# Kernel optimization log

Hardware: AMD Instinct MI355X
Metric: run time of the kernel (lower is better)

Reference implementation:

```python
import jax, jax.numpy as jnp
import numpy as np

N, E, IN, HID, H, C, L, NC = 10000, 60000, 768, 256, 8, 256, 4, 2
EPS, SLOPE = 1e-5, 0.2

def _ln(x, g, b):
    m = x.mean(-1, keepdims=True)
    v = x.var(-1, keepdims=True)
    return (x - m) / jnp.sqrt(v + EPS) * g + b

def _gelu(x):
    return jax.nn.gelu(x, approximate=False)  # torch nn.GELU default (erf)

def setup_inputs() -> dict:
    key = jax.random.key(0)
    ks = iter(jax.random.split(key, 40))
    def p(shape, s=0.02):
        return jax.random.normal(next(ks), shape, jnp.float32) * s
    return dict(
        x=jax.random.normal(next(ks), (N, IN), jnp.float32),
        edge_index=jax.random.randint(next(ks), (2, E), 0, N, dtype=jnp.int32),
        W_in=p((HID, IN)), b_in=jnp.zeros((HID,), jnp.float32),
        virtual_node=p((1, HID)),
        Wl=p((L, H * C, HID)), bl=jnp.zeros((L, H * C), jnp.float32),
        Wr=p((L, H * C, HID)), br=jnp.zeros((L, H * C), jnp.float32),
        att=p((L, H, C)), gbias=jnp.zeros((L, HID), jnp.float32),
        V1=p((L, 2 * HID, HID)), v1b=jnp.zeros((L, 2 * HID), jnp.float32),
        V2=p((L, HID, 2 * HID)), v2b=jnp.zeros((L, HID), jnp.float32),
        U1=p((L, 2 * HID, 2 * HID)), u1b=jnp.zeros((L, 2 * HID), jnp.float32),
        U2=p((L, HID, 2 * HID)), u2b=jnp.zeros((L, HID), jnp.float32),
        g1=jnp.ones((L, HID), jnp.float32), be1=jnp.zeros((L, HID), jnp.float32),
        g2=jnp.ones((L, HID), jnp.float32), be2=jnp.zeros((L, HID), jnp.float32),
        g3=jnp.ones((L, HID), jnp.float32), be3=jnp.zeros((L, HID), jnp.float32),
        O1=p((HID, HID)), o1b=jnp.zeros((HID,), jnp.float32),
        O2=p((NC, HID)), o2b=jnp.zeros((NC,), jnp.float32),
    )

def reference(x, edge_index, W_in, b_in, virtual_node, Wl, bl, Wr, br, att, gbias,
              V1, v1b, V2, v2b, U1, u1b, U2, u2b,
              g1, be1, g2, be2, g3, be3, O1, o1b, O2, o2b):
    # add self loops (PyG add_self_loops=True)
    loops = jnp.arange(N, dtype=edge_index.dtype)
    src = jnp.concatenate([edge_index[0], loops])  # message sources j
    dst = jnp.concatenate([edge_index[1], loops])  # message targets i

    x = x @ W_in.T + b_in                      # [N, HID]
    vn = virtual_node                          # [1, HID]
    for i in range(L):
        # --- GATv2Conv (concat=False -> mean over heads), eval mode (no dropout) ---
        xl = (x @ Wl[i].T + bl[i]).reshape(N, H, C)   # source transform
        xr = (x @ Wr[i].T + br[i]).reshape(N, H, C)   # target transform
        m = jax.nn.leaky_relu(xl[src] + xr[dst], SLOPE)       # [Etot, H, C]
        e = jnp.einsum('ehc,hc->eh', m, att[i])                # [Etot, H]
        emax = jax.ops.segment_max(e, dst, num_segments=N)
        a = jnp.exp(e - emax[dst])
        denom = jax.ops.segment_sum(a, dst, num_segments=N)
        alpha = a / denom[dst]                                  # segment softmax
        agg = jax.ops.segment_sum(xl[src] * alpha[:, :, None], dst, num_segments=N)
        x_local = agg.mean(axis=1) + gbias[i]                   # [N, HID]
        x = _ln(x + x_local, g1[i], be1[i])
        # --- virtual node update ---
        vn_in = x.mean(axis=0, keepdims=True)
        vn_up = _gelu(vn_in @ V1[i].T + v1b[i]) @ V2[i].T + v2b[i]
        vn = _ln(vn + vn_up, g2[i], be2[i])
        # --- node update with broadcast VN ---
        xc = jnp.concatenate([x, jnp.broadcast_to(vn, (N, HID))], axis=1)
        xu = _gelu(xc @ U1[i].T + u1b[i]) @ U2[i].T + u2b[i]
        x = _ln(x + xu, g3[i], be3[i])
    return _gelu(x @ O1.T + o1b) @ O2.T + o2b
```

## Files before the change

kernel.cpp:

```cpp
#include <hip/hip_runtime.h>
#include <hip/hip_bf16.h>
#include <cstdint>
#include <cstddef>

#define N_NODES 10000
#define M_PAD   10112
#define N_EDGES 60000
#define ETOT    70000
#define DIM_IN  768
#define HID     256
#define NHEAD   8
#define CH      256
#define HC      2048
#define NLAYER  4
#define NCLS    2
#define EPSLN   1e-5f
#define SLOPE   0.2f
#define DEG_CAP 128

typedef __bf16 bf16;
typedef __bf16 bf16x8 __attribute__((ext_vector_type(8)));
typedef float  f32x4  __attribute__((ext_vector_type(4)));

__device__ __forceinline__ float gelu_erf(float x) {
  return 0.5f * x * (1.0f + erff(x * 0.70710678118654752f));
}

__device__ __forceinline__ void gl2lds16(const void* g, void* l) {
  __builtin_amdgcn_global_load_lds(
      (const __attribute__((address_space(1))) unsigned int*)g,
      (__attribute__((address_space(3))) unsigned int*)l,
      16, 0, 0);
}

__global__ void k_count(const int* __restrict__ ei, int* __restrict__ deg) {
  int e = blockIdx.x * 256 + threadIdx.x;
  if (e >= ETOT) return;
  int d = (e < N_EDGES) ? ei[N_EDGES + e] : (e - N_EDGES);
  atomicAdd(&deg[d], 1);
}

__global__ void k_scan(const int* __restrict__ deg, int* __restrict__ offs) {
  __shared__ int lds[1024];
  const int t = threadIdx.x;
  const int c0 = t * 10;
  int s = 0;
  #pragma unroll
  for (int q = 0; q < 10; ++q) { int idx = c0 + q; if (idx < N_NODES) s += deg[idx]; }
  lds[t] = s;
  __syncthreads();
  for (int o = 1; o < 1024; o <<= 1) {
    int v = (t >= o) ? lds[t - o] : 0;
    __syncthreads();
    lds[t] += v;
    __syncthreads();
  }
  int run = lds[t] - s;
  #pragma unroll
  for (int q = 0; q < 10; ++q) {
    int idx = c0 + q;
    if (idx < N_NODES) { offs[idx] = run; run += deg[idx]; }
  }
  if (t == 1023) offs[N_NODES] = lds[1023];
}

__global__ void k_scatter(const int* __restrict__ ei, const int* __restrict__ offs,
                          int* __restrict__ fill, int* __restrict__ adj) {
  int e = blockIdx.x * 256 + threadIdx.x;
  if (e >= ETOT) return;
  int s, d;
  if (e < N_EDGES) { s = ei[e]; d = ei[N_EDGES + e]; } else { s = e - N_EDGES; d = s; }
  int pos = offs[d] + atomicAdd(&fill[d], 1);
  adj[pos] = s;
}

__global__ void k_init_vn(const float* __restrict__ vnode, float* __restrict__ vn_cur) {
  int t = threadIdx.x;
  if (t < HID) vn_cur[t] = vnode[t];
}

__global__ void k_f2b(const float* __restrict__ src, bf16* __restrict__ dst, int n4) {
  int i = blockIdx.x * 256 + threadIdx.x;
  int stride = gridDim.x * 256;
  for (; i < n4; i += stride) {
    float4 v = reinterpret_cast<const float4*>(src)[i];
    bf16 o0 = (bf16)v.x, o1 = (bf16)v.y, o2 = (bf16)v.z, o3 = (bf16)v.w;
    ushort4 pack;
    pack.x = __builtin_bit_cast(unsigned short, o0);
    pack.y = __builtin_bit_cast(unsigned short, o1);
    pack.z = __builtin_bit_cast(unsigned short, o2);
    pack.w = __builtin_bit_cast(unsigned short, o3);
    reinterpret_cast<ushort4*>(dst)[i] = pack;
  }
}

__global__ void k_catw(const float* __restrict__ Wl, const float* __restrict__ Wr,
                       bf16* __restrict__ out) {
  int idx = blockIdx.x * 256 + threadIdx.x;
  const int total8 = NLAYER * 4096 * 256 / 8;
  if (idx >= total8) return;
  size_t flat = (size_t)idx * 8;
  int i   = (int)(flat / (4096 * 256));
  int rem = (int)(flat % (4096 * 256));
  int r = rem >> 8;
  int k = rem & 255;
  const float* src = (r < 2048)
      ? Wl + (((size_t)i * 2048 + r) << 8) + k
      : Wr + (((size_t)i * 2048 + (r - 2048)) << 8) + k;
  const float4* p4 = reinterpret_cast<const float4*>(src);
  float4 u0 = p4[0], u1 = p4[1];
  bf16x8 ov;
  ov[0]=(bf16)u0.x; ov[1]=(bf16)u0.y; ov[2]=(bf16)u0.z; ov[3]=(bf16)u0.w;
  ov[4]=(bf16)u1.x; ov[5]=(bf16)u1.y; ov[6]=(bf16)u1.z; ov[7]=(bf16)u1.w;
  reinterpret_cast<bf16x8*>(out)[idx] = ov;
}

__global__ void k_catb(const float* __restrict__ bl, const float* __restrict__ br,
                       float* __restrict__ out) {
  int idx = blockIdx.x * 256 + threadIdx.x;
  if (idx >= NLAYER * 4096) return;
  int i = idx >> 12, r = idx & 4095;
  out[idx] = (r < 2048) ? bl[i * 2048 + r] : br[i * 2048 + (r - 2048)];
}

template<int ACT, bool WB, bool WF>
__global__ __launch_bounds__(256) void k_gemm2(
    const bf16* __restrict__ A, int lda,
    const bf16* __restrict__ W, int ldw,
    const float* __restrict__ bias,
    bf16* __restrict__ Cb, float* __restrict__ Cf, int ldc,
    int M, int K, int NT)
{
  __shared__ bf16 As[2][128 * 64];
  __shared__ bf16 Bs[2][128 * 64];
  const int t = threadIdx.x;
  const int nwg = gridDim.x;
  const int qq = nwg >> 3, rr = nwg & 7;
  const int xcd = blockIdx.x & 7, loc = blockIdx.x >> 3;
  const int wg = (xcd < rr) ? (xcd * (qq + 1) + loc)
                            : (rr * (qq + 1) + (xcd - rr) * qq + loc);
  const int bm = (wg / NT) * 128;
  const int bn = (wg % NT) * 128;
  const int l = t & 63, w = t >> 6;
  const int wm = (w >> 1) * 64, wn = (w & 1) * 64;
  const int lr = l & 15, lg = l >> 4;
  const int sr = t >> 3;
  const int ps = t & 7;

  f32x4 acc[4][4];
  #pragma unroll
  for (int a = 0; a < 4; ++a)
    #pragma unroll
    for (int b = 0; b < 4; ++b) acc[a][b] = (f32x4){0.f, 0.f, 0.f, 0.f};

  auto stage = [&](int buf, int k0) {
    #pragma unroll
    for (int q = 0; q < 4; ++q) {
      int r = q * 32 + sr;
      int ls = ps ^ (r & 7);
      gl2lds16(A + (size_t)(bm + r) * lda + k0 + ls * 8, &As[buf][r * 64 + ps * 8]);
    }
    #pragma unroll
    for (int q = 0; q < 4; ++q) {
      int r = q * 32 + sr;
      int ls = ps ^ (r & 7);
      gl2lds16(W + (size_t)(bn + r) * ldw + k0 + ls * 8, &Bs[buf][r * 64 + ps * 8]);
    }
  };

  const int nt = K >> 6;
  stage(0, 0);
  __syncthreads();
  for (int kt = 0; kt < nt; ++kt) {
    if (kt + 1 < nt) stage((kt + 1) & 1, (kt + 1) << 6);
    const bf16* Ab = As[kt & 1];
    const bf16* Bb = Bs[kt & 1];
    #pragma unroll
    for (int ks = 0; ks < 2; ++ks) {
      bf16x8 af[4], bfr[4];
      #pragma unroll
      for (int mt = 0; mt < 4; ++mt) {
        int row = wm + mt * 16 + lr;
        int slot = ks * 4 + lg;
        af[mt] = *reinterpret_cast<const bf16x8*>(&Ab[row * 64 + ((slot ^ (row & 7)) * 8)]);
      }
      #pragma unroll
      for (int nt2 = 0; nt2 < 4; ++nt2) {
        int row = wn + nt2 * 16 + lr;
        int slot = ks * 4 + lg;
        bfr[nt2] = *reinterpret_cast<const bf16x8*>(&Bb[row * 64 + ((slot ^ (row & 7)) * 8)]);
      }
      #pragma unroll
      for (int mt = 0; mt < 4; ++mt)
        #pragma unroll
        for (int nt2 = 0; nt2 < 4; ++nt2)
          acc[mt][nt2] = __builtin_amdgcn_mfma_f32_16x16x32_bf16(af[mt], bfr[nt2], acc[mt][nt2], 0, 0, 0);
    }
    __syncthreads();
  }
  #pragma unroll
  for (int mt = 0; mt < 4; ++mt) {
    #pragma unroll
    for (int nt2 = 0; nt2 < 4; ++nt2) {
      int col = bn + wn + nt2 * 16 + lr;
      float bv = bias[col];
      #pragma unroll
      for (int j = 0; j < 4; ++j) {
        int row = bm + wm + mt * 16 + lg * 4 + j;
        if (row < M) {
          float vv = acc[mt][nt2][j] + bv;
          if (ACT == 1) vv = gelu_erf(vv);
          if (WB) Cb[(size_t)row * ldc + col] = (bf16)vv;
          if (WF) Cf[(size_t)row * ldc + col] = vv;
        }
      }
    }
  }
}

__global__ __launch_bounds__(256) void k_node_attn(
    float* __restrict__ x, bf16* __restrict__ xb,
    const bf16* __restrict__ xlr,
    const int* __restrict__ offs, const int* __restrict__ adj,
    const float* __restrict__ att_l, const float* __restrict__ gbias_l,
    const float* __restrict__ g_l, const float* __restrict__ b_l)
{
  __shared__ int   s_src[DEG_CAP];
  __shared__ float s_agg[HC];
  __shared__ float s_red[8];

  const int t = threadIdx.x;
  const int i = blockIdx.x;
  const int start = offs[i];
  int deg = offs[i + 1] - start;
  if (deg > DEG_CAP) deg = DEG_CAP;

  for (int j = t; j < deg; j += 256) s_src[j] = adj[start + j];

  float xr_reg[8], att_reg[8];
  {
    bf16x8 xv = *reinterpret_cast<const bf16x8*>(xlr + (size_t)i * 4096 + 2048 + 8 * t);
    #pragma unroll
    for (int q = 0; q < 8; ++q) xr_reg[q] = (float)xv[q];
    const float4* ap = reinterpret_cast<const float4*>(att_l + 8 * t);
    float4 a0 = ap[0], a1 = ap[1];
    att_reg[0]=a0.x; att_reg[1]=a0.y; att_reg[2]=a0.z; att_reg[3]=a0.w;
    att_reg[4]=a1.x; att_reg[5]=a1.y; att_reg[6]=a1.z; att_reg[7]=a1.w;
  }
  __syncthreads();

  float m = -1e30f, ssum = 0.f;
  float acc[8];
  #pragma unroll
  for (int q = 0; q < 8; ++q) acc[q] = 0.f;

  for (int j = 0; j < deg; ++j) {
    bf16x8 xv = *reinterpret_cast<const bf16x8*>(xlr + (size_t)s_src[j] * 4096 + 8 * t);
    float xf[8];
    float p = 0.f;
    #pragma unroll
    for (int q = 0; q < 8; ++q) {
      xf[q] = (float)xv[q];
      float z = xf[q] + xr_reg[q];
      z = (z > 0.f) ? z : SLOPE * z;
      p = fmaf(att_reg[q], z, p);
    }
    #pragma unroll
    for (int o = 16; o >= 1; o >>= 1) p += __shfl_xor(p, o, 32);
    if (__any(p > m)) {
      float mn = fmaxf(m, p);
      float scale = __expf(m - mn);
      ssum *= scale;
      #pragma unroll
      for (int q = 0; q < 8; ++q) acc[q] *= scale;
      m = mn;
    }
    float a = __expf(p - m);
    ssum += a;
    #pragma unroll
    for (int q = 0; q < 8; ++q) acc[q] = fmaf(a, xf[q], acc[q]);
  }
  float inv = 1.0f / ssum;
  #pragma unroll
  for (int q = 0; q < 8; ++q) s_agg[8 * t + q] = acc[q] * inv;
  __syncthreads();

  float xloc = 0.f;
  #pragma unroll
  for (int hh = 0; hh < NHEAD; ++hh) xloc += s_agg[hh * CH + t];
  xloc = xloc * (1.0f / NHEAD) + gbias_l[t];
  float r = x[(size_t)i * HID + t] + xloc;

  float s1 = r, s2 = r * r;
  #pragma unroll
  for (int o = 32; o >= 1; o >>= 1) { s1 += __shfl_xor(s1, o); s2 += __shfl_xor(s2, o); }
  if ((t & 63) == 0) { s_red[t >> 6] = s1; s_red[4 + (t >> 6)] = s2; }
  __syncthreads();
  s1 = s_red[0] + s_red[1] + s_red[2] + s_red[3];
  s2 = s_red[4] + s_red[5] + s_red[6] + s_red[7];
  float mean = s1 * (1.0f / HID);
  float var  = s2 * (1.0f / HID) - mean * mean;
  float o = (r - mean) * rsqrtf(var + EPSLN) * g_l[t] + b_l[t];
  x [(size_t)i * HID + t] = o;
  xb[(size_t)i * HID + t] = (bf16)o;
}

__global__ void k_colmean(const float* __restrict__ x, float* __restrict__ accum) {
  const int t = threadIdx.x, b = blockIdx.x;
  float s = 0.f;
  for (int r = b * 50; r < (b + 1) * 50; ++r) s += x[(size_t)r * HID + t];
  atomicAdd(&accum[t], s);
}

__global__ void k_vn_gemv1(const float* __restrict__ vn_accum,
                           const float* __restrict__ V1, const float* __restrict__ v1b,
                           float* __restrict__ z1) {
  const int o = blockIdx.x * 8 + (threadIdx.x >> 5);
  const int lane = threadIdx.x & 31;
  const float4* vp = reinterpret_cast<const float4*>(vn_accum + lane * 8);
  float4 a0 = vp[0], a1 = vp[1];
  const float4* wp = reinterpret_cast<const float4*>(V1 + (size_t)o * 256 + lane * 8);
  float4 w0 = wp[0], w1 = wp[1];
  float p = a0.x*w0.x + a0.y*w0.y + a0.z*w0.z + a0.w*w0.w
          + a1.x*w1.x + a1.y*w1.y + a1.z*w1.z + a1.w*w1.w;
  #pragma unroll
  for (int s = 16; s >= 1; s >>= 1) p += __shfl_xor(p, s, 32);
  if (lane == 0) z1[o] = gelu_erf(p * (1.0f / (float)N_NODES) + v1b[o]);
}

__global__ void k_vn_gemv2(const float* __restrict__ z1,
                           const float* __restrict__ V2, const float* __restrict__ v2b,
                           float* __restrict__ vn_up) {
  const int o = blockIdx.x * 8 + (threadIdx.x >> 5);
  const int lane = threadIdx.x & 31;
  float p = 0.f;
  #pragma unroll
  for (int c = 0; c < 4; ++c) {
    float4 a = reinterpret_cast<const float4*>(z1 + lane * 16)[c];
    float4 w = reinterpret_cast<const float4*>(V2 + (size_t)o * 512 + lane * 16)[c];
    p += a.x*w.x + a.y*w.y + a.z*w.z + a.w*w.w;
  }
  #pragma unroll
  for (int s = 16; s >= 1; s >>= 1) p += __shfl_xor(p, s, 32);
  if (lane == 0) vn_up[o] = p + v2b[o];
}

__global__ void k_vn_ln(float* __restrict__ vn_cur, const float* __restrict__ vn_up,
                        const float* __restrict__ g2, const float* __restrict__ be2) {
  __shared__ float s_red[8];
  const int t = threadIdx.x;
  float r = vn_cur[t] + vn_up[t];
  float s1 = r, s2 = r * r;
  #pragma unroll
  for (int o = 32; o >= 1; o >>= 1) { s1 += __shfl_xor(s1, o); s2 += __shfl_xor(s2, o); }
  if ((t & 63) == 0) { s_red[t >> 6] = s1; s_red[4 + (t >> 6)] = s2; }
  __syncthreads();
  s1 = s_red[0] + s_red[1] + s_red[2] + s_red[3];
  s2 = s_red[4] + s_red[5] + s_red[6] + s_red[7];
  float mean = s1 * (1.0f / HID);
  float var  = s2 * (1.0f / HID) - mean * mean;
  vn_cur[t] = (r - mean) * rsqrtf(var + EPSLN) * g2[t] + be2[t];
}

__global__ void k_vn_ctr(const float* __restrict__ vn_cur,
                         const float* __restrict__ U1, const float* __restrict__ u1b,
                         float* __restrict__ vn_ctr) {
  const int o = blockIdx.x * 8 + (threadIdx.x >> 5);
  const int lane = threadIdx.x & 31;
  const float4* vp = reinterpret_cast<const float4*>(vn_cur + lane * 8);
  float4 a0 = vp[0], a1 = vp[1];
  const float4* wp = reinterpret_cast<const float4*>(U1 + (size_t)o * 512 + 256 + lane * 8);
  float4 w0 = wp[0], w1 = wp[1];
  float p = a0.x*w0.x + a0.y*w0.y + a0.z*w0.z + a0.w*w0.w
          + a1.x*w1.x + a1.y*w1.y + a1.z*w1.z + a1.w*w1.w;
  #pragma unroll
  for (int s = 16; s >= 1; s >>= 1) p += __shfl_xor(p, s, 32);
  if (lane == 0) vn_ctr[o] = p + u1b[o];
}

__global__ __launch_bounds__(256) void k_ln_res(
    float* __restrict__ x, bf16* __restrict__ xb, const float* __restrict__ xu,
    const float* __restrict__ g_l, const float* __restrict__ b_l)
{
  __shared__ float s_red[8];
  const int t = threadIdx.x, i = blockIdx.x;
  float r = x[(size_t)i * HID + t] + xu[(size_t)i * HID + t];
  float s1 = r, s2 = r * r;
  #pragma unroll
  for (int o = 32; o >= 1; o >>= 1) { s1 += __shfl_xor(s1, o); s2 += __shfl_xor(s2, o); }
  if ((t & 63) == 0) { s_red[t >> 6] = s1; s_red[4 + (t >> 6)] = s2; }
  __syncthreads();
  s1 = s_red[0] + s_red[1] + s_red[2] + s_red[3];
  s2 = s_red[4] + s_red[5] + s_red[6] + s_red[7];
  float mean = s1 * (1.0f / HID);
  float var  = s2 * (1.0f / HID) - mean * mean;
  float o = (r - mean) * rsqrtf(var + EPSLN) * g_l[t] + b_l[t];
  x [(size_t)i * HID + t] = o;
  xb[(size_t)i * HID + t] = (bf16)o;
}

__global__ void k_final(const float* __restrict__ g, const float* __restrict__ O2,
                        const float* __restrict__ o2b, float* __restrict__ out) {
  int tid = blockIdx.x * 256 + threadIdx.x;
  if (tid >= N_NODES * NCLS) return;
  int n = tid >> 1, j = tid & 1;
  const float* gr = g + (size_t)n * HID;
  const float* w  = O2 + (size_t)j * HID;
  float d = o2b[j];
  for (int k = 0; k < HID; ++k) d = fmaf(gr[k], w[k], d);
  out[tid] = d;
}

extern "C" void kernel_launch(void* const* d_in, const int* in_sizes, int n_in,
                              void* d_out, int out_size, void* d_ws, size_t ws_size,
                              hipStream_t stream)
{
  const float* x_in  = (const float*)d_in[0];
  const int*   ei    = (const int*)  d_in[1];
  const float* W_in  = (const float*)d_in[2];
  const float* b_in  = (const float*)d_in[3];
  const float* vnode = (const float*)d_in[4];
  const float* Wl    = (const float*)d_in[5];
  const float* bl    = (const float*)d_in[6];
  const float* Wr    = (const float*)d_in[7];
  const float* br    = (const float*)d_in[8];
  const float* att   = (const float*)d_in[9];
  const float* gbias = (const float*)d_in[10];
  const float* V1    = (const float*)d_in[11];
  const float* v1b   = (const float*)d_in[12];
  const float* V2    = (const float*)d_in[13];
  const float* v2b   = (const float*)d_in[14];
  const float* U1    = (const float*)d_in[15];
  const float* u1b   = (const float*)d_in[16];
  const float* U2    = (const float*)d_in[17];
  const float* u2b   = (const float*)d_in[18];
  const float* g1    = (const float*)d_in[19];
  const float* be1   = (const float*)d_in[20];
  const float* g2    = (const float*)d_in[21];
  const float* be2   = (const float*)d_in[22];
  const float* g3    = (const float*)d_in[23];
  const float* be3   = (const float*)d_in[24];
  const float* O1    = (const float*)d_in[25];
  const float* o1b   = (const float*)d_in[26];
  const float* O2    = (const float*)d_in[27];
  const float* o2b   = (const float*)d_in[28];
  float* out = (float*)d_out;

  char* ws = (char*)d_ws;
  size_t cur = 0;
  auto alloc = [&](size_t bytes) -> char* {
    char* p = ws + cur;
    cur = (cur + bytes + 255) & ~(size_t)255;
    return p;
  };
  float* x        = (float*)alloc((size_t)M_PAD * HID * 4);
  bf16*  xb       = (bf16*) alloc((size_t)M_PAD * HID * 2);
  bf16*  xlr      = (bf16*) alloc((size_t)M_PAD * 4096 * 2);
  bf16*  h1       = (bf16*) alloc((size_t)M_PAD * 2 * HID * 2);
  float* xu       = (float*)alloc((size_t)M_PAD * HID * 4);
  bf16*  Wlrb     = (bf16*) alloc((size_t)NLAYER * 4096 * HID * 2);
  float* blr      = (float*)alloc((size_t)NLAYER * 4096 * 4);
  bf16*  U1b      = (bf16*) alloc((size_t)NLAYER * 2 * HID * 2 * HID * 2);
  bf16*  U2b      = (bf16*) alloc((size_t)NLAYER * HID * 2 * HID * 2);
  bf16*  O1b      = (bf16*) alloc((size_t)HID * HID * 2);
  bf16*  Winb     = (bf16*) alloc((size_t)HID * DIM_IN * 2);
  int*   deg      = (int*)  alloc((size_t)N_NODES * 4);
  int*   offs     = (int*)  alloc((size_t)(N_NODES + 1) * 4);
  int*   fill     = (int*)  alloc((size_t)N_NODES * 4);
  int*   adj      = (int*)  alloc((size_t)ETOT * 4);
  float* vn_accum = (float*)alloc(HID * 4);
  float* vn_cur   = (float*)alloc(HID * 4);
  float* vn_ctr   = (float*)alloc(2 * HID * 4);
  float* z1buf    = (float*)alloc(2 * HID * 4);
  float* vn_up    = (float*)alloc(HID * 4);

  bf16* x_in_b = xlr;

  hipMemsetAsync(deg, 0, (size_t)N_NODES * 4, stream);
  hipMemsetAsync(fill, 0, (size_t)N_NODES * 4, stream);
  k_count<<<(ETOT + 255) / 256, 256, 0, stream>>>(ei, deg);
  k_scan<<<1, 1024, 0, stream>>>(deg, offs);
  k_scatter<<<(ETOT + 255) / 256, 256, 0, stream>>>(ei, offs, fill, adj);
  k_init_vn<<<1, 256, 0, stream>>>(vnode, vn_cur);

  k_catw<<<(NLAYER * 4096 * 256 / 8 + 255) / 256, 256, 0, stream>>>(Wl, Wr, Wlrb);
  k_catb<<<(NLAYER * 4096 + 255) / 256, 256, 0, stream>>>(bl, br, blr);
  k_f2b<<<256, 256, 0, stream>>>(U1, U1b, NLAYER * 2 * HID * 2 * HID / 4);
  k_f2b<<<128, 256, 0, stream>>>(U2, U2b, NLAYER * HID * 2 * HID / 4);
  k_f2b<<<64, 256, 0, stream>>>(O1, O1b, HID * HID / 4);
  k_f2b<<<64, 256, 0, stream>>>(W_in, Winb, HID * DIM_IN / 4);
  k_f2b<<<512, 256, 0, stream>>>(x_in, x_in_b, N_NODES * DIM_IN / 4);

  const int MT = M_PAD / 128;

  k_gemm2<0, true, true><<<MT * 2, 256, 0, stream>>>(
      x_in_b, DIM_IN, Winb, DIM_IN, b_in, xb, x, HID, N_NODES, DIM_IN, 2);

  for (int i = 0; i < NLAYER; ++i) {
    const bf16* Wlrb_i = Wlrb + (size_t)i * 4096 * HID;
    const bf16* U1b_i  = U1b + (size_t)i * 2 * HID * 2 * HID;
    const bf16* U2b_i  = U2b + (size_t)i * HID * 2 * HID;

    k_gemm2<0, true, false><<<MT * 32, 256, 0, stream>>>(
        xb, HID, Wlrb_i, HID, blr + (size_t)i * 4096, xlr, nullptr, 4096, N_NODES, HID, 32);

    k_node_attn<<<N_NODES, 256, 0, stream>>>(x, xb, xlr, offs, adj,
        att + (size_t)i * HC, gbias + (size_t)i * HID,
        g1 + (size_t)i * HID, be1 + (size_t)i * HID);

    hipMemsetAsync(vn_accum, 0, HID * 4, stream);
    k_colmean<<<200, 256, 0, stream>>>(x, vn_accum);
    k_vn_gemv1<<<64, 256, 0, stream>>>(vn_accum,
        V1 + (size_t)i * 2 * HID * HID, v1b + (size_t)i * 2 * HID, z1buf);
    k_vn_gemv2<<<32, 256, 0, stream>>>(z1buf,
        V2 + (size_t)i * HID * 2 * HID, v2b + (size_t)i * HID, vn_up);
    k_vn_ln<<<1, 256, 0, stream>>>(vn_cur, vn_up,
        g2 + (size_t)i * HID, be2 + (size_t)i * HID);
    k_vn_ctr<<<64, 256, 0, stream>>>(vn_cur,
        U1 + (size_t)i * 2 * HID * 2 * HID, u1b + (size_t)i * 2 * HID, vn_ctr);

    k_gemm2<1, true, false><<<MT * 4, 256, 0, stream>>>(
        xb, HID, U1b_i, 2 * HID, vn_ctr, h1, nullptr, 2 * HID, N_NODES, HID, 4);
    k_gemm2<0, false, true><<<MT * 2, 256, 0, stream>>>(
        h1, 2 * HID, U2b_i, 2 * HID, u2b + (size_t)i * HID, nullptr, xu, HID, N_NODES, 2 * HID, 2);

    k_ln_res<<<N_NODES, 256, 0, stream>>>(x, xb, xu, g3 + (size_t)i * HID, be3 + (size_t)i * HID);
  }

  k_gemm2<1, false, true><<<MT * 2, 256, 0, stream>>>(
      xb, HID, O1b, HID, o1b, nullptr, xu, HID, N_NODES, HID, 2);
  k_final<<<(N_NODES * NCLS + 255) / 256, 256, 0, stream>>>(xu, O2, o2b, out);
}
```

Before: 971.9 us.

## Add 64x64 GEMM for narrow outputs, finer waitcnt pipelining, branchless leaky-relu

Adds a 64x64-tile GEMM variant and routes the narrow-output GEMMs (input projection, U1, U2, output head) to it. This raises the workgroup count on the 256-CU part, where 128x128 tiles left only about 158–316 blocks. Both GEMMs replace __syncthreads with explicit vmcnt waits and raw barriers, so the prefetch of the next K tile overlaps the current compute. The attention kernel rewrites leaky-relu times att as 0.6*a*z + 0.4*a*|z| to avoid the select. The trade-offs are less data reuse per tile and hand-tuned waitcnt counts that depend on the exact number of loads.

```diff
diff --git a/kernel.cpp b/kernel.cpp
--- a/kernel.cpp
+++ b/kernel.cpp
@@ -170,9 +170,15 @@
 
   const int nt = K >> 6;
   stage(0, 0);
-  __syncthreads();
   for (int kt = 0; kt < nt; ++kt) {
-    if (kt + 1 < nt) stage((kt + 1) & 1, (kt + 1) << 6);
+    if (kt + 1 < nt) {
+      stage((kt + 1) & 1, (kt + 1) << 6);
+      asm volatile("s_waitcnt vmcnt(8)" ::: "memory");
+    } else {
+      asm volatile("s_waitcnt vmcnt(0)" ::: "memory");
+    }
+    __builtin_amdgcn_s_barrier();
+    asm volatile("" ::: "memory");
     const bf16* Ab = As[kt & 1];
     const bf16* Bb = Bs[kt & 1];
     #pragma unroll
@@ -196,12 +202,117 @@
         for (int nt2 = 0; nt2 < 4; ++nt2)
           acc[mt][nt2] = __builtin_amdgcn_mfma_f32_16x16x32_bf16(af[mt], bfr[nt2], acc[mt][nt2], 0, 0, 0);
     }
-    __syncthreads();
+    asm volatile("" ::: "memory");
+    __builtin_amdgcn_s_barrier();
+    asm volatile("" ::: "memory");
   }
   #pragma unroll
   for (int mt = 0; mt < 4; ++mt) {
     #pragma unroll
     for (int nt2 = 0; nt2 < 4; ++nt2) {
+      int col = bn + wn + nt2 * 16 + lr;
+      float bv = bias[col];
+      #pragma unroll
+      for (int j = 0; j < 4; ++j) {
+        int row = bm + wm + mt * 16 + lg * 4 + j;
+        if (row < M) {
+          float vv = acc[mt][nt2][j] + bv;
+          if (ACT == 1) vv = gelu_erf(vv);
+          if (WB) Cb[(size_t)row * ldc + col] = (bf16)vv;
+          if (WF) Cf[(size_t)row * ldc + col] = vv;
+        }
+      }
+    }
+  }
+}
+
+template<int ACT, bool WB, bool WF>
+__global__ __launch_bounds__(256) void k_gemm64(
+    const bf16* __restrict__ A, int lda,
+    const bf16* __restrict__ W, int ldw,
+    const float* __restrict__ bias,
+    bf16* __restrict__ Cb, float* __restrict__ Cf, int ldc,
+    int M, int K, int NT)
+{
+  __shared__ bf16 As[2][64 * 64];
+  __shared__ bf16 Bs[2][64 * 64];
+  const int t = threadIdx.x;
+  const int nwg = gridDim.x;
+  const int qq = nwg >> 3, rr = nwg & 7;
+  const int xcd = blockIdx.x & 7, loc = blockIdx.x >> 3;
+  const int wg = (xcd < rr) ? (xcd * (qq + 1) + loc)
+                            : (rr * (qq + 1) + (xcd - rr) * qq + loc);
+  const int bm = (wg / NT) * 64;
+  const int bn = (wg % NT) * 64;
+  const int l = t & 63, w = t >> 6;
+  const int wm = (w >> 1) * 32, wn = (w & 1) * 32;
+  const int lr = l & 15, lg = l >> 4;
+  const int sr = t >> 3;
+  const int ps = t & 7;
+
+  f32x4 acc[2][2];
+  #pragma unroll
+  for (int a = 0; a < 2; ++a)
+    #pragma unroll
+    for (int b = 0; b < 2; ++b) acc[a][b] = (f32x4){0.f, 0.f, 0.f, 0.f};
+
+  auto stage = [&](int buf, int k0) {
+    #pragma unroll
+    for (int q = 0; q < 2; ++q) {
+      int r = q * 32 + sr;
+      int ls = ps ^ (r & 7);
+      gl2lds16(A + (size_t)(bm + r) * lda + k0 + ls * 8, &As[buf][r * 64 + ps * 8]);
+    }
+    #pragma unroll
+    for (int q = 0; q < 2; ++q) {
+      int r = q * 32 + sr;
+      int ls = ps ^ (r & 7);
+      gl2lds16(W + (size_t)(bn + r) * ldw + k0 + ls * 8, &Bs[buf][r * 64 + ps * 8]);
+    }
+  };
+
+  const int nt = K >> 6;
+  stage(0, 0);
+  for (int kt = 0; kt < nt; ++kt) {
+    if (kt + 1 < nt) {
+      stage((kt + 1) & 1, (kt + 1) << 6);
+      asm volatile("s_waitcnt vmcnt(4)" ::: "memory");
+    } else {
+      asm volatile("s_waitcnt vmcnt(0)" ::: "memory");
+    }
+    __builtin_amdgcn_s_barrier();
+    asm volatile("" ::: "memory");
+    const bf16* Ab = As[kt & 1];
+    const bf16* Bb = Bs[kt & 1];
+    #pragma unroll
+    for (int ks = 0; ks < 2; ++ks) {
+      bf16x8 af[2], bfr[2];
+      #pragma unroll
+      for (int mt = 0; mt < 2; ++mt) {
+        int row = wm + mt * 16 + lr;
+        int slot = ks * 4 + lg;
+        af[mt] = *reinterpret_cast<const bf16x8*>(&Ab[row * 64 + ((slot ^ (row & 7)) * 8)]);
+      }
+      #pragma unroll
+      for (int nt2 = 0; nt2 < 2; ++nt2) {
+        int row = wn + nt2 * 16 + lr;
+        int slot = ks * 4 + lg;
+        bfr[nt2] = *reinterpret_cast<const bf16x8*>(&Bb[row * 64 + ((slot ^ (row & 7)) * 8)]);
+      }
+      #pragma unroll
+      for (int mt = 0; mt < 2; ++mt)
+        #pragma unroll
+        for (int nt2 = 0; nt2 < 2; ++nt2)
+          acc[mt][nt2] = __builtin_amdgcn_mfma_f32_16x16x32_bf16(af[mt], bfr[nt2], acc[mt][nt2], 0, 0, 0);
+    }
+    asm volatile("" ::: "memory");
+    __builtin_amdgcn_s_barrier();
+    asm volatile("" ::: "memory");
+  }
+  #pragma unroll
+  for (int mt = 0; mt < 2; ++mt) {
+    #pragma unroll
+    for (int nt2 = 0; nt2 < 2; ++nt2) {
       int col = bn + wn + nt2 * 16 + lr;
       float bv = bias[col];
       #pragma unroll
@@ -237,15 +348,17 @@
 
   for (int j = t; j < deg; j += 256) s_src[j] = adj[start + j];
 
-  float xr_reg[8], att_reg[8];
+  float xr_reg[8], a6[8], a4[8];
   {
     bf16x8 xv = *reinterpret_cast<const bf16x8*>(xlr + (size_t)i * 4096 + 2048 + 8 * t);
     #pragma unroll
     for (int q = 0; q < 8; ++q) xr_reg[q] = (float)xv[q];
     const float4* ap = reinterpret_cast<const float4*>(att_l + 8 * t);
     float4 a0 = ap[0], a1 = ap[1];
-    att_reg[0]=a0.x; att_reg[1]=a0.y; att_reg[2]=a0.z; att_reg[3]=a0.w;
-    att_reg[4]=a1.x; att_reg[5]=a1.y; att_reg[6]=a1.z; att_reg[7]=a1.w;
+    a6[0]=0.6f*a0.x; a6[1]=0.6f*a0.y; a6[2]=0.6f*a0.z; a6[3]=0.6f*a0.w;
+    a6[4]=0.6f*a1.x; a6[5]=0.6f*a1.y; a6[6]=0.6f*a1.z; a6[7]=0.6f*a1.w;
+    a4[0]=0.4f*a0.x; a4[1]=0.4f*a0.y; a4[2]=0.4f*a0.z; a4[3]=0.4f*a0.w;
+    a4[4]=0.4f*a1.x; a4[5]=0.4f*a1.y; a4[6]=0.4f*a1.z; a4[7]=0.4f*a1.w;
   }
   __syncthreads();
 
@@ -262,8 +375,8 @@
     for (int q = 0; q < 8; ++q) {
       xf[q] = (float)xv[q];
       float z = xf[q] + xr_reg[q];
-      z = (z > 0.f) ? z : SLOPE * z;
-      p = fmaf(att_reg[q], z, p);
+      p = fmaf(a6[q], z, p);
+      p = fmaf(a4[q], fabsf(z), p);
     }
     #pragma unroll
     for (int o = 16; o >= 1; o >>= 1) p += __shfl_xor(p, o, 32);
@@ -491,10 +604,11 @@
   k_f2b<<<64, 256, 0, stream>>>(W_in, Winb, HID * DIM_IN / 4);
   k_f2b<<<512, 256, 0, stream>>>(x_in, x_in_b, N_NODES * DIM_IN / 4);
 
-  const int MT = M_PAD / 128;
-
-  k_gemm2<0, true, true><<<MT * 2, 256, 0, stream>>>(
-      x_in_b, DIM_IN, Winb, DIM_IN, b_in, xb, x, HID, N_NODES, DIM_IN, 2);
+  const int MT64 = M_PAD / 64;
+  const int MT   = M_PAD / 128;
+
+  k_gemm64<0, true, true><<<MT64 * 4, 256, 0, stream>>>(
+      x_in_b, DIM_IN, Winb, DIM_IN, b_in, xb, x, HID, N_NODES, DIM_IN, 4);
 
   for (int i = 0; i < NLAYER; ++i) {
     const bf16* Wlrb_i = Wlrb + (size_t)i * 4096 * HID;
@@ -519,15 +633,15 @@
     k_vn_ctr<<<64, 256, 0, stream>>>(vn_cur,
         U1 + (size_t)i * 2 * HID * 2 * HID, u1b + (size_t)i * 2 * HID, vn_ctr);
 
-    k_gemm2<1, true, false><<<MT * 4, 256, 0, stream>>>(
-        xb, HID, U1b_i, 2 * HID, vn_ctr, h1, nullptr, 2 * HID, N_NODES, HID, 4);
-    k_gemm2<0, false, true><<<MT * 2, 256, 0, stream>>>(
-        h1, 2 * HID, U2b_i, 2 * HID, u2b + (size_t)i * HID, nullptr, xu, HID, N_NODES, 2 * HID, 2);
+    k_gemm64<1, true, false><<<MT64 * 8, 256, 0, stream>>>(
+        xb, HID, U1b_i, 2 * HID, vn_ctr, h1, nullptr, 2 * HID, N_NODES, HID, 8);
+    k_gemm64<0, false, true><<<MT64 * 4, 256, 0, stream>>>(
+        h1, 2 * HID, U2b_i, 2 * HID, u2b + (size_t)i * HID, nullptr, xu, HID, N_NODES, 2 * HID, 4);
 
     k_ln_res<<<N_NODES, 256, 0, stream>>>(x, xb, xu, g3 + (size_t)i * HID, be3 + (size_t)i * HID);
   }
 
-  k_gemm2<1, false, true><<<MT * 2, 256, 0, stream>>>(
-      xb, HID, O1b, HID, o1b, nullptr, xu, HID, N_NODES, HID, 2);
+  k_gemm64<1, false, true><<<MT64 * 4, 256, 0, stream>>>(
+      xb, HID, O1b, HID, o1b, nullptr, xu, HID, N_NODES, HID, 4);
   k_final<<<(N_NODES * NCLS + 255) / 256, 256, 0, stream>>>(xu, O2, o2b, out);
 }
```

Result: no change. 968.4 us (-0.4%).
